# Kernel tuning notes

Hardware: AMD Instinct MI355X
Metric: run time of the kernel (lower is better)

The kernel has to match this reference:

```python
import jax, jax.numpy as jnp
import numpy as np

NTOKENS = 8192
H = 1024
FFN = 2048
NEXPERTS = 64
TOPK = 2
M = NTOKENS * TOPK  # total routed slots


def setup_inputs() -> dict:
    key = jax.random.key(0)
    k1, k2, k3 = jax.random.split(key, 3)
    inputs_shard = jax.random.normal(k1, (NTOKENS, H), dtype=jnp.float32)
    w1 = jax.random.normal(k2, (NEXPERTS, H, FFN), dtype=jnp.float32) * 0.02
    w2 = jax.random.normal(k3, (NEXPERTS, FFN, H), dtype=jnp.float32) * 0.02
    # Balanced routing: each expert receives exactly M // NEXPERTS slots.
    rng = np.random.default_rng(0)
    per_expert = M // NEXPERTS
    eid_flat = rng.permutation(np.repeat(np.arange(M // per_expert), per_expert))  # [M] expert id per (token,k)
    order = np.argsort(eid_flat, kind='stable')  # slot -> flat (token,k) index
    scatter_flat = np.empty(M, dtype=np.int64)
    scatter_flat[order] = np.arange(M)  # (token,k) -> slot in expert-sorted buffer
    scatter_index = jnp.asarray(scatter_flat.reshape(NTOKENS, TOPK))
    splits = jnp.full((NEXPERTS,), per_expert, dtype=jnp.int64)
    return {"inputs_shard": inputs_shard, "w1": w1, "w2": w2,
            "scatter_index": scatter_index, "splits": splits}


def reference(inputs_shard, w1, w2, scatter_index, splits):
    ntokens, topk = scatter_index.shape
    m = ntokens * topk
    nexperts = w1.shape[0]
    per_expert = m // nexperts  # splits are balanced by construction
    # AG-scatter: place each token copy into its expert-sorted slot.
    slot_to_tk = jnp.argsort(scatter_index.reshape(-1))  # slot -> (token,k) flat idx
    token = slot_to_tk // topk                            # slot -> source token
    expanded = inputs_shard[token]                        # [M, H]
    # Grouped GEMM 1 (h -> ffn) + exact gelu, per expert block.
    xg = expanded.reshape(nexperts, per_expert, -1)       # [G, M/G, H]
    h1 = jnp.einsum('geh,ghf->gef', xg, w1)               # [G, M/G, FFN]
    a = jax.nn.gelu(h1, approximate=False)
    # Grouped GEMM 2 (ffn -> h).
    h2 = jnp.einsum('gef,gfh->geh', a, w2).reshape(m, -1)  # [M, H]
    # Gather-RS: gather topk partials per token and reduce (sum).
    out = h2[scatter_index.reshape(-1)].reshape(ntokens, topk, -1).sum(axis=1)
    return out
```

## Files before the change

kernel.cpp:

```cpp
#include <hip/hip_runtime.h>
#include <hip/hip_bf16.h>
#include <math.h>

#define NTOK 8192
#define HD   1024
#define FFND 2048
#define NE   64
#define MTOT 16384
#define PER_E 256

typedef __attribute__((ext_vector_type(8))) short bh8;
typedef __attribute__((ext_vector_type(4))) float f4;
typedef unsigned short u16;
typedef unsigned int   u32;

__device__ __forceinline__ u16 f2bf(float f) {
  union { float f; u32 u; } x; x.f = f;
  u32 r = x.u + 0x7fffu + ((x.u >> 16) & 1u);
  return (u16)(r >> 16);
}

__device__ __forceinline__ float bf2f(u16 b) {
  union { u32 u; float f; } x; x.u = ((u32)b) << 16; return x.f;
}

__device__ __forceinline__ u32 pk2(float lo, float hi) {
  __hip_bfloat162 h = __float22bfloat162_rn(make_float2(lo, hi));
  union { __hip_bfloat162 h; u32 u; } c; c.h = h;
  return c.u;
}

__global__ void k_build_s2t(const int* __restrict__ sidx, int* __restrict__ s2t) {
  int i = blockIdx.x * 256 + threadIdx.x;
  s2t[sidx[i]] = i >> 1;
}

__global__ void k_gather_x(const float* __restrict__ inp, const int* __restrict__ s2t,
                           u16* __restrict__ X) {
  int idx = blockIdx.x * 256 + threadIdx.x;
  int slot = idx >> 7;
  int c    = idx & 127;
  const float* src = inp + (size_t)s2t[slot] * HD + c * 8;
  float v[8];
  *(f4*)(v)     = *(const f4*)(src);
  *(f4*)(v + 4) = *(const f4*)(src + 4);
  u32 o[4];
  #pragma unroll
  for (int j = 0; j < 4; ++j) o[j] = pk2(v[2 * j], v[2 * j + 1]);
  *(uint4*)(X + (size_t)slot * HD + c * 8) = *(uint4*)o;
}

template<int K, int N, int BN, bool GELU>
__global__ __launch_bounds__(512, 4)
void moe_gemm(const u16* __restrict__ Abf, const float* __restrict__ Bf,
              u16* __restrict__ outp)
{
  constexpr int BM = 256, BK = 64;
  constexpr int NB = N / BN;
  constexpr int NT = K / BK;
  constexpr int NF = BN / 32;
  constexpr int BITER = BN / 64;
  constexpr int ABYTES = BM * 128;
  __shared__ __align__(16) char lds[2 * ABYTES + BN * 128];
  char* Bs = lds + 2 * ABYTES;

  const int d = blockIdx.y * NB + blockIdx.x;
  const int x = d & 7, j = d >> 3;
  const int e  = x * (NE / 8) + j / NB;
  const int n0 = (j % NB) * BN;
  const int row0 = e * PER_E;
  const int tid  = threadIdx.x;
  const int lane = tid & 63, wid = tid >> 6;
  const int wr   = wid >> 1, wc = wid & 1;

  const u16*   Arow = Abf + (size_t)row0 * K;
  const float* Bsrc = Bf + (size_t)e * K * N + n0;

  auto stageA = [&](int buf, int k0) {
    char* dst = lds + buf * ABYTES;
    #pragma unroll
    for (int i = 0; i < 4; ++i) {
      int c = i * 512 + tid;
      int r = c >> 3, kc = c & 7;
      int kswz = kc ^ (r & 7);
      __builtin_amdgcn_global_load_lds(
          (const void*)(Arow + (size_t)r * K + k0 + kswz * 8),
          (void*)(dst + c * 16), 16, 0, 0);
    }
  };
  auto loadB = [&](float* br, int k0) {
    #pragma unroll
    for (int i = 0; i < BITER; ++i) {
      int c = i * 512 + tid;
      int n = c & (BN - 1), kc = c / BN;
      const float* p = Bsrc + (size_t)(k0 + kc * 8) * N + n;
      #pragma unroll
      for (int jj = 0; jj < 8; ++jj) br[i * 8 + jj] = p[(size_t)jj * N];
    }
  };
  auto writeB = [&](const float* br) {
    #pragma unroll
    for (int i = 0; i < BITER; ++i) {
      int c = i * 512 + tid;
      int n = c & (BN - 1), kc = c / BN;
      u32 q[4];
      #pragma unroll
      for (int jj = 0; jj < 4; ++jj) q[jj] = pk2(br[i * 8 + 2 * jj], br[i * 8 + 2 * jj + 1]);
      *(uint4*)(Bs + n * 128 + ((kc * 16) ^ ((n & 7) << 4))) = *(uint4*)q;
    }
  };

  f4 acc[4][NF] = {};
  float breg[BITER * 8];

  stageA(0, 0);
  loadB(breg, 0);
  writeB(breg);
  asm volatile("s_waitcnt vmcnt(0) lgkmcnt(0)" ::: "memory");
  __builtin_amdgcn_sched_barrier(0);
  __builtin_amdgcn_s_barrier();
  __builtin_amdgcn_sched_barrier(0);

  int cur = 0;
  for (int t = 0; t < NT; ++t) {
    const char* As = lds + cur * ABYTES;
    if (t + 1 < NT) {
      stageA(cur ^ 1, (t + 1) * BK);
      loadB(breg, (t + 1) * BK);
    }
    __builtin_amdgcn_s_setprio(1);
    #pragma unroll
    for (int kk = 0; kk < 2; ++kk) {
      int kByte = kk * 64 + ((lane >> 4) << 4);
      bh8 a[4], b[NF];
      #pragma unroll
      for (int m = 0; m < 4; ++m) {
        int r = wr * 64 + m * 16 + (lane & 15);
        a[m] = *(const bh8*)(As + r * 128 + (kByte ^ ((r & 7) << 4)));
      }
      #pragma unroll
      for (int n = 0; n < NF; ++n) {
        int r = wc * (NF * 16) + n * 16 + (lane & 15);
        b[n] = *(const bh8*)(Bs + r * 128 + (kByte ^ ((r & 7) << 4)));
      }
      #pragma unroll
      for (int m = 0; m < 4; ++m)
        #pragma unroll
        for (int n = 0; n < NF; ++n)
          acc[m][n] = __builtin_amdgcn_mfma_f32_16x16x32_bf16(a[m], b[n], acc[m][n], 0, 0, 0);
    }
    __builtin_amdgcn_s_setprio(0);
    __builtin_amdgcn_s_barrier();
    __builtin_amdgcn_sched_barrier(0);
    if (t + 1 < NT) {
      writeB(breg);
      asm volatile("s_waitcnt vmcnt(0) lgkmcnt(0)" ::: "memory");
      __builtin_amdgcn_sched_barrier(0);
      __builtin_amdgcn_s_barrier();
      __builtin_amdgcn_sched_barrier(0);
      cur ^= 1;
    }
  }

  #pragma unroll
  for (int m = 0; m < 4; ++m) {
    #pragma unroll
    for (int n = 0; n < NF; ++n) {
      int rowb = wr * 64 + m * 16 + ((lane >> 4) << 2);
      int col  = n0 + wc * (NF * 16) + n * 16 + (lane & 15);
      #pragma unroll
      for (int jj = 0; jj < 4; ++jj) {
        float xv = acc[m][n][jj];
        if (GELU) {
          float y = fminf(fmaxf(xv, -8.f), 8.f);
          float u = 0.7978845608f * (y + 0.044715f * y * y * y);
          float t2 = __expf(-2.f * u);
          float g = __fdividef(y, 1.f + t2);
          outp[(size_t)(row0 + rowb + jj) * N + col] = f2bf(g);
        } else {
          outp[(size_t)(row0 + rowb + jj) * N + col] = f2bf(xv);
        }
      }
    }
  }
}

__global__ void k_reduce(const u16* __restrict__ h2, const int* __restrict__ sidx,
                         float* __restrict__ out) {
  int t = blockIdx.x;
  int c = threadIdx.x;
  const u16* r0 = h2 + (size_t)sidx[2 * t] * HD + c * 4;
  const u16* r1 = h2 + (size_t)sidx[2 * t + 1] * HD + c * 4;
  u16 a0[4], a1[4];
  *(uint2*)a0 = *(const uint2*)r0;
  *(uint2*)a1 = *(const uint2*)r1;
  f4 s;
  #pragma unroll
  for (int jj = 0; jj < 4; ++jj) s[jj] = bf2f(a0[jj]) + bf2f(a1[jj]);
  *(f4*)(out + (size_t)t * HD + c * 4) = s;
}

extern "C" void kernel_launch(void* const* d_in, const int* in_sizes, int n_in,
                              void* d_out, int out_size, void* d_ws, size_t ws_size,
                              hipStream_t stream) {
  const float* inp  = (const float*)d_in[0];
  const float* w1   = (const float*)d_in[1];
  const float* w2   = (const float*)d_in[2];
  const int*   sidx = (const int*)d_in[3];
  float* out = (float*)d_out;

  char* ws   = (char*)d_ws;
  int*   s2t = (int*)ws;
  u16*   X   = (u16*)(ws + (1 << 20));
  u16*   act = (u16*)(ws + (1 << 20) + (32u << 20));
  u16*   h2  = (u16*)(ws + (1 << 20) + (96u << 20));

  k_build_s2t<<<MTOT / 256, 256, 0, stream>>>(sidx, s2t);
  k_gather_x<<<(MTOT * (HD / 8)) / 256, 256, 0, stream>>>(inp, s2t, X);
  moe_gemm<HD, FFND, 128, true><<<dim3(FFND / 128, NE), 512, 0, stream>>>(X, w1, act);
  moe_gemm<FFND, HD, 64, false><<<dim3(HD / 64, NE), 512, 0, stream>>>(act, w2, h2);
  k_reduce<<<NTOK, 256, 0, stream>>>(h2, sidx, out);
}
```

Measured before the change: 314.0 us.

## Widen GEMM N-tile to 256 and use partial vmcnt waits for B prefetch

Both grouped GEMMs now use a 256x256 output tile per block, with launch bounds lowered to 2 blocks per CU, and the grid shrinks to match. B loads are issued before the A global-to-LDS copies, and partial s_waitcnt vmcnt counts wait only for the B register loads rather than draining every outstanding load. The aim is fewer re-reads of A and more overlap of the fp32 weight loads with MFMA work. The cost is much higher register pressure (8x8 accumulator fragments), lower occupancy, and far fewer blocks for the second GEMM (256 blocks), which may underfill the GPU.

```diff
diff --git a/kernel.cpp b/kernel.cpp
--- a/kernel.cpp
+++ b/kernel.cpp
@@ -50,16 +50,16 @@
   *(uint4*)(X + (size_t)slot * HD + c * 8) = *(uint4*)o;
 }
 
-template<int K, int N, int BN, bool GELU>
-__global__ __launch_bounds__(512, 4)
+template<int K, int N, bool GELU>
+__global__ __launch_bounds__(512, 2)
 void moe_gemm(const u16* __restrict__ Abf, const float* __restrict__ Bf,
               u16* __restrict__ outp)
 {
-  constexpr int BM = 256, BK = 64;
+  constexpr int BM = 256, BN = 256, BK = 64;
   constexpr int NB = N / BN;
   constexpr int NT = K / BK;
-  constexpr int NF = BN / 32;
-  constexpr int BITER = BN / 64;
+  constexpr int NF = 8;
+  constexpr int BITER = 4;
   constexpr int ABYTES = BM * 128;
   __shared__ __align__(16) char lds[2 * ABYTES + BN * 128];
   char* Bs = lds + 2 * ABYTES;
@@ -113,10 +113,13 @@
   f4 acc[4][NF] = {};
   float breg[BITER * 8];
 
+  loadB(breg, 0);
+  __builtin_amdgcn_sched_barrier(0);
   stageA(0, 0);
-  loadB(breg, 0);
+  asm volatile("s_waitcnt vmcnt(4)" ::: "memory");
+  __builtin_amdgcn_sched_barrier(0);
   writeB(breg);
-  asm volatile("s_waitcnt vmcnt(0) lgkmcnt(0)" ::: "memory");
+  asm volatile("s_waitcnt lgkmcnt(0)" ::: "memory");
   __builtin_amdgcn_sched_barrier(0);
   __builtin_amdgcn_s_barrier();
   __builtin_amdgcn_sched_barrier(0);
@@ -125,9 +128,14 @@
   for (int t = 0; t < NT; ++t) {
     const char* As = lds + cur * ABYTES;
     if (t + 1 < NT) {
+      loadB(breg, (t + 1) * BK);
+      __builtin_amdgcn_sched_barrier(0);
       stageA(cur ^ 1, (t + 1) * BK);
-      loadB(breg, (t + 1) * BK);
-    }
+      asm volatile("s_waitcnt vmcnt(36)" ::: "memory");
+    } else {
+      asm volatile("s_waitcnt vmcnt(0)" ::: "memory");
+    }
+    __builtin_amdgcn_sched_barrier(0);
     __builtin_amdgcn_s_setprio(1);
     #pragma unroll
     for (int kk = 0; kk < 2; ++kk) {
@@ -140,7 +148,7 @@
       }
       #pragma unroll
       for (int n = 0; n < NF; ++n) {
-        int r = wc * (NF * 16) + n * 16 + (lane & 15);
+        int r = wc * 128 + n * 16 + (lane & 15);
         b[n] = *(const bh8*)(Bs + r * 128 + (kByte ^ ((r & 7) << 4)));
       }
       #pragma unroll
@@ -153,8 +161,10 @@
     __builtin_amdgcn_s_barrier();
     __builtin_amdgcn_sched_barrier(0);
     if (t + 1 < NT) {
+      asm volatile("s_waitcnt vmcnt(4)" ::: "memory");
+      __builtin_amdgcn_sched_barrier(0);
       writeB(breg);
-      asm volatile("s_waitcnt vmcnt(0) lgkmcnt(0)" ::: "memory");
+      asm volatile("s_waitcnt lgkmcnt(0)" ::: "memory");
       __builtin_amdgcn_sched_barrier(0);
       __builtin_amdgcn_s_barrier();
       __builtin_amdgcn_sched_barrier(0);
@@ -167,7 +177,7 @@
     #pragma unroll
     for (int n = 0; n < NF; ++n) {
       int rowb = wr * 64 + m * 16 + ((lane >> 4) << 2);
-      int col  = n0 + wc * (NF * 16) + n * 16 + (lane & 15);
+      int col  = n0 + wc * 128 + n * 16 + (lane & 15);
       #pragma unroll
       for (int jj = 0; jj < 4; ++jj) {
         float xv = acc[m][n][jj];
@@ -217,7 +227,7 @@
 
   k_build_s2t<<<MTOT / 256, 256, 0, stream>>>(sidx, s2t);
   k_gather_x<<<(MTOT * (HD / 8)) / 256, 256, 0, stream>>>(inp, s2t, X);
-  moe_gemm<HD, FFND, 128, true><<<dim3(FFND / 128, NE), 512, 0, stream>>>(X, w1, act);
-  moe_gemm<FFND, HD, 64, false><<<dim3(HD / 64, NE), 512, 0, stream>>>(act, w2, h2);
+  moe_gemm<HD, FFND, true><<<dim3(FFND / 256, NE), 512, 0, stream>>>(X, w1, act);
+  moe_gemm<FFND, HD, false><<<dim3(HD / 256, NE), 512, 0, stream>>>(act, w2, h2);
   k_reduce<<<NTOK, 256, 0, stream>>>(h2, sidx, out);
 }
```

Measured after the change: 292.3 us. 6.9% less time.
